# Optimization experiments

Measured on AMD Instinct MI355X. Metric: run time of the kernel, lower is better.

## Reference

```python
import jax, jax.numpy as jnp
import numpy as np

HIDDEN = 1024
STATE = 16
DT_RANK = 64


def setup_inputs() -> dict:
    key = jax.random.key(0)
    ks = jax.random.split(key, 5)
    B, S = 2, 2048
    x = jax.random.normal(ks[0], (B, S, HIDDEN), dtype=jnp.float32)
    # lecun_normal-ish init scales
    W_xproj = jax.random.normal(ks[1], (HIDDEN, STATE * 2 + DT_RANK), dtype=jnp.float32) / np.sqrt(HIDDEN)
    W_dt = jax.random.normal(ks[2], (DT_RANK, HIDDEN), dtype=jnp.float32) / np.sqrt(DT_RANK)
    b_dt = jnp.zeros((HIDDEN,), dtype=jnp.float32)
    A_log = jax.random.normal(ks[3], (STATE, HIDDEN), dtype=jnp.float32) / np.sqrt(STATE)
    return {"x": x, "W_xproj": W_xproj, "W_dt": W_dt, "b_dt": b_dt, "A_log": A_log}


def reference(x, W_xproj, W_dt, b_dt, A_log):
    # x: [B, S, D]
    xp = x @ W_xproj                       # [B, S, 2N + R]
    Bm = xp[..., :STATE]                    # [B, S, N]
    Cm = xp[..., STATE:2 * STATE]           # [B, S, N]
    dt = jax.nn.softplus(xp[..., 2 * STATE:] @ W_dt + b_dt)  # [B, S, D]
    A = -jnp.exp(A_log)                     # [N, D]
    A_bar = jnp.exp(A[None, None] * dt[:, :, None, :])        # [B, S, N, D]
    Bu = Bm[:, :, :, None] * dt[:, :, None, :] * x[:, :, None, :]  # [B, S, N, D]

    def scan_fn(h, inp):
        A_t, Bu_t = inp
        h = A_t * h + Bu_t
        return h, h

    h0 = jnp.zeros(Bu.shape[:1] + Bu.shape[2:], dtype=x.dtype)   # [B, N, D]
    _, h_all = jax.lax.scan(scan_fn, h0,
                            (A_bar.transpose(1, 0, 2, 3), Bu.transpose(1, 0, 2, 3)))  # [S, B, N, D]
    y = jnp.einsum('bsn,sbnd->bsd', Cm, h_all)  # [B, S, D]
    return y
```

## Files before the change

### kernel.cpp

```cpp
#include <hip/hip_runtime.h>
#include <math.h>

#define HIDDEN 1024
#define NSTATE 16
#define DTRANK 64
#define BB 2
#define SS 2048
#define ROWS (BB*SS)
#define XPC 96
#define CH 128
#define CL 16
#define BND (BB*NSTATE*HIDDEN)
#define LOG2E 1.44269504088896f

#define RT 64
#define KSPL 8

__global__ __launch_bounds__(256) void k_xproj2(const float* __restrict__ x,
                                                const float* __restrict__ W,
                                                float* __restrict__ part) {
    __shared__ float xs[RT * 32];
    __shared__ float wt[96 * 36];
    int t  = threadIdx.x;
    int rt = blockIdx.x >> 3;
    int ks = blockIdx.x & 7;
    int r0 = rt * RT;
    int k0 = ks * 128;
    int cg = t & 15, rg = t >> 4;

    float acc[4][6];
    #pragma unroll
    for (int a = 0; a < 4; ++a)
        #pragma unroll
        for (int b = 0; b < 6; ++b) acc[a][b] = 0.f;

    for (int ch = 0; ch < 4; ++ch) {
        int kc = k0 + ch * 32;
        __syncthreads();
        #pragma unroll
        for (int m = 0; m < 2; ++m) {
            int e = t + m * 256;
            int row = e >> 3, kb = e & 7;
            float4 v = *(const float4*)&x[(r0 + row) * HIDDEN + kc + kb * 4];
            int kbp = kb ^ ((row >> 2) & 7);
            *(float4*)&xs[row * 32 + kbp * 4] = v;
        }
        #pragma unroll
        for (int m = 0; m < 3; ++m) {
            int f = t + m * 256;
            int kr = f / 24, cq = f % 24;
            float4 v = *(const float4*)&W[(kc + kr) * XPC + cq * 4];
            wt[(cq * 4 + 0) * 36 + kr] = v.x;
            wt[(cq * 4 + 1) * 36 + kr] = v.y;
            wt[(cq * 4 + 2) * 36 + kr] = v.z;
            wt[(cq * 4 + 3) * 36 + kr] = v.w;
        }
        __syncthreads();
        #pragma unroll
        for (int kg = 0; kg < 8; ++kg) {
            float4 wv[6], xv[4];
            #pragma unroll
            for (int j = 0; j < 6; ++j)
                wv[j] = *(float4*)&wt[(cg + 16 * j) * 36 + kg * 4];
            #pragma unroll
            for (int rr = 0; rr < 4; ++rr) {
                int row = rg * 4 + rr;
                xv[rr] = *(float4*)&xs[row * 32 + ((kg ^ ((row >> 2) & 7)) * 4)];
            }
            #pragma unroll
            for (int rr = 0; rr < 4; ++rr)
                #pragma unroll
                for (int j = 0; j < 6; ++j) {
                    acc[rr][j] = fmaf(xv[rr].x, wv[j].x, acc[rr][j]);
                    acc[rr][j] = fmaf(xv[rr].y, wv[j].y, acc[rr][j]);
                    acc[rr][j] = fmaf(xv[rr].z, wv[j].z, acc[rr][j]);
                    acc[rr][j] = fmaf(xv[rr].w, wv[j].w, acc[rr][j]);
                }
        }
    }
    #pragma unroll
    for (int rr = 0; rr < 4; ++rr)
        #pragma unroll
        for (int j = 0; j < 6; ++j)
            part[ks * (ROWS * XPC) + (r0 + rg * 4 + rr) * XPC + cg + 16 * j] = acc[rr][j];
}

__global__ void k_rdt(const float* __restrict__ part, const float* __restrict__ Wdt,
                      const float* __restrict__ bdt, float* __restrict__ xp,
                      float* __restrict__ dt) {
    __shared__ float xs[8 * 64];
    int t = threadIdx.x;
    int r0 = blockIdx.x * 8;
    #pragma unroll
    for (int m = 0; m < 3; ++m) {
        int o = t + m * 256;
        int row = o / 96, col = o % 96;
        float s = 0.f;
        #pragma unroll
        for (int p = 0; p < KSPL; ++p)
            s += part[p * (ROWS * XPC) + (r0 + row) * XPC + col];
        xp[(r0 + row) * XPC + col] = s;
        if (col >= 2 * NSTATE) xs[row * 64 + (col - 2 * NSTATE)] = s;
    }
    __syncthreads();
    float4 acc[8];
    float4 b = *(const float4*)&bdt[t * 4];
    #pragma unroll
    for (int rr = 0; rr < 8; ++rr) acc[rr] = b;
    #pragma unroll 4
    for (int k = 0; k < DTRANK; ++k) {
        float4 w = *(const float4*)&Wdt[k * HIDDEN + t * 4];
        #pragma unroll
        for (int rr = 0; rr < 8; ++rr) {
            float s = xs[rr * 64 + k];
            acc[rr].x = fmaf(s, w.x, acc[rr].x);
            acc[rr].y = fmaf(s, w.y, acc[rr].y);
            acc[rr].z = fmaf(s, w.z, acc[rr].z);
            acc[rr].w = fmaf(s, w.w, acc[rr].w);
        }
    }
    #pragma unroll
    for (int rr = 0; rr < 8; ++rr) {
        float4 a = acc[rr], o;
        o.x = fmaxf(a.x, 0.f) + log1pf(__expf(-fabsf(a.x)));
        o.y = fmaxf(a.y, 0.f) + log1pf(__expf(-fabsf(a.y)));
        o.z = fmaxf(a.z, 0.f) + log1pf(__expf(-fabsf(a.z)));
        o.w = fmaxf(a.w, 0.f) + log1pf(__expf(-fabsf(a.w)));
        *(float4*)&dt[(r0 + rr) * HIDDEN + t * 4] = o;
    }
}

__global__ __launch_bounds__(256, 4)
void k_pass1(const float* __restrict__ x, const float* __restrict__ dt,
             const float* __restrict__ xp, const float* __restrict__ Alog,
             float* __restrict__ P, float* __restrict__ Q) {
    int bid = blockIdx.x;
    int dblk = bid & 3;
    int b = (bid >> 2) & 1;
    int c = bid >> 3;
    int d = dblk * 256 + threadIdx.x;
    float A2[NSTATE], Pv[NSTATE], Qv[NSTATE];
    #pragma unroll
    for (int n = 0; n < NSTATE; ++n) {
        A2[n] = -__expf(Alog[n*HIDDEN + d]) * LOG2E;
        Pv[n] = 1.f; Qv[n] = 0.f;
    }
    int s0 = c * CL;
    #pragma unroll 4
    for (int i = 0; i < CL; ++i) {
        int r = b*SS + s0 + i;
        float dv = dt[r*HIDDEN + d];
        float xv = x[r*HIDDEN + d];
        float bm[NSTATE];
        *(float4*)&bm[0]  = *(const float4*)&xp[r*XPC + 0];
        *(float4*)&bm[4]  = *(const float4*)&xp[r*XPC + 4];
        *(float4*)&bm[8]  = *(const float4*)&xp[r*XPC + 8];
        *(float4*)&bm[12] = *(const float4*)&xp[r*XPC + 12];
        float bx = dv * xv;
        #pragma unroll
        for (int n = 0; n < NSTATE; ++n) {
            float a = exp2f(A2[n] * dv);
            Qv[n] = fmaf(a, Qv[n], bm[n] * bx);
            Pv[n] *= a;
        }
    }
    int base = b*(NSTATE*HIDDEN) + d;
    #pragma unroll
    for (int n = 0; n < NSTATE; ++n) {
        P[c*BND + base + n*HIDDEN] = Pv[n];
        Q[c*BND + base + n*HIDDEN] = Qv[n];
    }
}

__global__ void k_pass2(float* __restrict__ P, const float* __restrict__ Q) {
    int bnd = blockIdx.x * 256 + threadIdx.x;
    float h = 0.f;
    for (int cb = 0; cb < CH / 16; ++cb) {
        float p[16], q[16];
        #pragma unroll
        for (int j = 0; j < 16; ++j) {
            int idx = (cb*16 + j)*BND + bnd;
            p[j] = P[idx]; q[j] = Q[idx];
        }
        #pragma unroll
        for (int j = 0; j < 16; ++j) {
            int idx = (cb*16 + j)*BND + bnd;
            P[idx] = h;
            h = fmaf(p[j], h, q[j]);
        }
    }
}

__global__ __launch_bounds__(256, 4)
void k_pass3(const float* __restrict__ x, const float* __restrict__ dt,
             const float* __restrict__ xp, const float* __restrict__ Alog,
             const float* __restrict__ Hs, float* __restrict__ y) {
    int bid = blockIdx.x;
    int dblk = bid & 3;
    int b = (bid >> 2) & 1;
    int c = bid >> 3;
    int d = dblk * 256 + threadIdx.x;

    float A2[NSTATE], h[NSTATE];
    #pragma unroll
    for (int n = 0; n < NSTATE; ++n) {
        A2[n] = -__expf(Alog[n*HIDDEN + d]) * LOG2E;
        h[n] = Hs[c*BND + b*(NSTATE*HIDDEN) + n*HIDDEN + d];
    }
    int s0 = c * CL;
    #pragma unroll 2
    for (int i = 0; i < CL; ++i) {
        int r = b*SS + s0 + i;
        float dv = dt[r*HIDDEN + d];
        float xv = x[r*HIDDEN + d];
        float bx = dv * xv;
        float bm[NSTATE], cm[NSTATE];
        *(float4*)&bm[0]  = *(const float4*)&xp[r*XPC + 0];
        *(float4*)&bm[4]  = *(const float4*)&xp[r*XPC + 4];
        *(float4*)&bm[8]  = *(const float4*)&xp[r*XPC + 8];
        *(float4*)&bm[12] = *(const float4*)&xp[r*XPC + 12];
        *(float4*)&cm[0]  = *(const float4*)&xp[r*XPC + 16];
        *(float4*)&cm[4]  = *(const float4*)&xp[r*XPC + 20];
        *(float4*)&cm[8]  = *(const float4*)&xp[r*XPC + 24];
        *(float4*)&cm[12] = *(const float4*)&xp[r*XPC + 28];
        float yv = 0.f;
        #pragma unroll
        for (int n = 0; n < NSTATE; ++n) {
            float a = exp2f(A2[n] * dv);
            h[n] = fmaf(a, h[n], bm[n] * bx);
            yv = fmaf(cm[n], h[n], yv);
        }
        y[r*HIDDEN + d] = yv;
    }
}

extern "C" void kernel_launch(void* const* d_in, const int* in_sizes, int n_in,
                              void* d_out, int out_size, void* d_ws, size_t ws_size,
                              hipStream_t stream) {
    const float* x    = (const float*)d_in[0];
    const float* Wx   = (const float*)d_in[1];
    const float* Wdt  = (const float*)d_in[2];
    const float* bdt  = (const float*)d_in[3];
    const float* Alog = (const float*)d_in[4];
    float* y  = (float*)d_out;
    float* ws = (float*)d_ws;

    float* xp   = ws;
    float* dt   = xp + ROWS*XPC;
    float* part = dt + ROWS*HIDDEN;
    float* P    = part + (size_t)KSPL*ROWS*XPC;
    float* Q    = P + (size_t)CH*BND;

    k_xproj2<<<(ROWS/RT)*KSPL, 256, 0, stream>>>(x, Wx, part);
    k_rdt<<<ROWS/8, 256, 0, stream>>>(part, Wdt, bdt, xp, dt);
    k_pass1<<<CH*BB*4, 256, 0, stream>>>(x, dt, xp, Alog, P, Q);
    k_pass2<<<BND/256, 256, 0, stream>>>(P, Q);
    k_pass3<<<CH*BB*4, 256, 0, stream>>>(x, dt, xp, Alog, P, y);
}
```

Measured before the change: 112.4 us.

## Split split-K reduction from dt projection and widen dt grid per column

The fused reduce-plus-dt kernel becomes two kernels. The first is a vectorized float4 reduction of the split-K partials into xp. The second computes the dt projection with one output column per thread, over four times as many blocks, and uses a fast __logf instead of log1pf in the softplus. The aim is to raise parallelism and memory coalescing in the dt stage and make the reduction cheaper. In exchange it adds a kernel launch and an extra round trip of xp through global memory, and __logf(1+e) loses accuracy for large |a|.

```diff
diff --git a/kernel.cpp b/kernel.cpp
--- a/kernel.cpp
+++ b/kernel.cpp
@@ -15,6 +15,7 @@
 
 #define RT 64
 #define KSPL 8
+#define RX (ROWS*XPC)
 
 __global__ __launch_bounds__(256) void k_xproj2(const float* __restrict__ x,
                                                 const float* __restrict__ W,
@@ -82,51 +83,50 @@
     for (int rr = 0; rr < 4; ++rr)
         #pragma unroll
         for (int j = 0; j < 6; ++j)
-            part[ks * (ROWS * XPC) + (r0 + rg * 4 + rr) * XPC + cg + 16 * j] = acc[rr][j];
-}
-
-__global__ void k_rdt(const float* __restrict__ part, const float* __restrict__ Wdt,
-                      const float* __restrict__ bdt, float* __restrict__ xp,
-                      float* __restrict__ dt) {
+            part[ks * RX + (r0 + rg * 4 + rr) * XPC + cg + 16 * j] = acc[rr][j];
+}
+
+__global__ void k_reduce(const float* __restrict__ part, float* __restrict__ xp) {
+    int i = (blockIdx.x * 256 + threadIdx.x) * 4;
+    float4 s = *(const float4*)&part[i];
+    #pragma unroll
+    for (int p = 1; p < KSPL; ++p) {
+        float4 v = *(const float4*)&part[p * RX + i];
+        s.x += v.x; s.y += v.y; s.z += v.z; s.w += v.w;
+    }
+    *(float4*)&xp[i] = s;
+}
+
+__global__ __launch_bounds__(256) void k_dt3(const float* __restrict__ xp,
+                                             const float* __restrict__ Wdt,
+                                             const float* __restrict__ bdt,
+                                             float* __restrict__ dt) {
     __shared__ float xs[8 * 64];
     int t = threadIdx.x;
-    int r0 = blockIdx.x * 8;
-    #pragma unroll
-    for (int m = 0; m < 3; ++m) {
-        int o = t + m * 256;
-        int row = o / 96, col = o % 96;
-        float s = 0.f;
-        #pragma unroll
-        for (int p = 0; p < KSPL; ++p)
-            s += part[p * (ROWS * XPC) + (r0 + row) * XPC + col];
-        xp[(r0 + row) * XPC + col] = s;
-        if (col >= 2 * NSTATE) xs[row * 64 + (col - 2 * NSTATE)] = s;
+    int r0 = (blockIdx.x >> 2) * 8;
+    int col = (blockIdx.x & 3) * 256 + t;
+    if (t < 128) {
+        int row = t >> 4, kq = t & 15;
+        *(float4*)&xs[row * 64 + kq * 4] =
+            *(const float4*)&xp[(r0 + row) * XPC + 2 * NSTATE + kq * 4];
     }
     __syncthreads();
-    float4 acc[8];
-    float4 b = *(const float4*)&bdt[t * 4];
+    float acc[8];
+    float b = bdt[col];
     #pragma unroll
     for (int rr = 0; rr < 8; ++rr) acc[rr] = b;
-    #pragma unroll 4
+    #pragma unroll 8
     for (int k = 0; k < DTRANK; ++k) {
-        float4 w = *(const float4*)&Wdt[k * HIDDEN + t * 4];
-        #pragma unroll
-        for (int rr = 0; rr < 8; ++rr) {
-            float s = xs[rr * 64 + k];
-            acc[rr].x = fmaf(s, w.x, acc[rr].x);
-            acc[rr].y = fmaf(s, w.y, acc[rr].y);
-            acc[rr].z = fmaf(s, w.z, acc[rr].z);
-            acc[rr].w = fmaf(s, w.w, acc[rr].w);
-        }
+        float w = Wdt[k * HIDDEN + col];
+        #pragma unroll
+        for (int rr = 0; rr < 8; ++rr)
+            acc[rr] = fmaf(xs[rr * 64 + k], w, acc[rr]);
     }
     #pragma unroll
     for (int rr = 0; rr < 8; ++rr) {
-        float4 a = acc[rr], o;
-        o.x = fmaxf(a.x, 0.f) + log1pf(__expf(-fabsf(a.x)));
-        o.y = fmaxf(a.y, 0.f) + log1pf(__expf(-fabsf(a.y)));
-        o.z = fmaxf(a.z, 0.f) + log1pf(__expf(-fabsf(a.z)));
-        o.w = fmaxf(a.w, 0.f) + log1pf(__expf(-fabsf(a.w)));
-        *(float4*)&dt[(r0 + rr) * HIDDEN + t * 4] = o;
+        float a = acc[rr];
+        float o = fmaxf(a, 0.f) + __logf(1.f + __expf(-fabsf(a)));
+        dt[(r0 + rr) * HIDDEN + col] = o;
     }
 }
 
@@ -246,13 +246,14 @@
     float* ws = (float*)d_ws;
 
     float* xp   = ws;
-    float* dt   = xp + ROWS*XPC;
+    float* dt   = xp + RX;
     float* part = dt + ROWS*HIDDEN;
-    float* P    = part + (size_t)KSPL*ROWS*XPC;
+    float* P    = part + (size_t)KSPL*RX;
     float* Q    = P + (size_t)CH*BND;
 
     k_xproj2<<<(ROWS/RT)*KSPL, 256, 0, stream>>>(x, Wx, part);
-    k_rdt<<<ROWS/8, 256, 0, stream>>>(part, Wdt, bdt, xp, dt);
+    k_reduce<<<RX/4/256, 256, 0, stream>>>(part, xp);
+    k_dt3<<<(ROWS/8)*4, 256, 0, stream>>>(xp, Wdt, bdt, dt);
     k_pass1<<<CH*BB*4, 256, 0, stream>>>(x, dt, xp, Alog, P, Q);
     k_pass2<<<BND/256, 256, 0, stream>>>(P, Q);
     k_pass3<<<CH*BB*4, 256, 0, stream>>>(x, dt, xp, Alog, P, y);
```

Result: slower. 116.9 us (+4.0%).
